# Optimization experiments

Measured on AMD Instinct MI355X. Metric: run time of the kernel, lower is better.

The kernel has to match this reference:

```python
import jax, jax.numpy as jnp
import numpy as np

B, N, D, H = 2, 2048, 1024, 16
HD = D // H  # head_dim = 64


def l2norm(x, eps=1e-12):
    n = jnp.sqrt(jnp.sum(x * x, axis=-1, keepdims=True))
    return x / jnp.maximum(n, eps)


def setup_inputs() -> dict:
    key = jax.random.key(0)
    ks = jax.random.split(key, 10)
    s = 0.02
    return {
        "x": jax.random.normal(ks[0], (B, N, D), jnp.float32),
        "Wq": jax.random.normal(ks[1], (D, D), jnp.float32) * s,
        "Wk": jax.random.normal(ks[2], (D, D), jnp.float32) * s,
        "Wv": jax.random.normal(ks[3], (D, D), jnp.float32) * s,
        "Wgamma": jax.random.normal(ks[4], (D, H), jnp.float32) * s,
        "Wf": jax.random.normal(ks[5], (D, H), jnp.float32) * s,
        "Wg1": jax.random.normal(ks[6], (D, HD), jnp.float32) * s,
        "Wg2": jax.random.normal(ks[7], (HD, D), jnp.float32) * s,
        "Wo": jax.random.normal(ks[8], (D, D), jnp.float32) * s,
        "norm_w": jnp.ones((D,), jnp.float32),
    }


def dplr_delta_rule(q, k, v, a, gk):
    # q,k,v,a,gk: (B,N,H,HD). State S: (B,H,Dk,Dv). b-vector == k here.
    # S' = S * exp(gk_t); S_t = S' + k_t (x) (a_t @ S' + v_t); o_t = q_t @ S_t
    qm, km, vm, am, gm = (jnp.moveaxis(t, 1, 0) for t in (q, k, v, a, gk))

    def step(S, inp):
        qt, kt, vt, at, gkt = inp  # (B,H,HD)
        Sp = S * jnp.exp(gkt)[..., None]
        u = jnp.einsum('bhk,bhkv->bhv', at, Sp) + vt
        S = Sp + jnp.einsum('bhk,bhv->bhkv', kt, u)
        o = jnp.einsum('bhk,bhkv->bhv', qt, S)
        return S, o

    S0 = jnp.zeros((q.shape[0], q.shape[2], q.shape[3], v.shape[3]), q.dtype)
    _, o = jax.lax.scan(step, S0, (qm, km, vm, am, gm))
    return jnp.moveaxis(o, 0, 1)  # (B,N,H,HD)


def _forward(x, Wq, Wk, Wv, Wgamma, Wf, Wg1, Wg2, Wo, norm_w):
    b, n, d = x.shape
    silu = jax.nn.silu
    q = silu(x @ Wq)
    k = silu(x @ Wk)
    v = silu(x @ Wv)
    log_f = jax.nn.log_sigmoid(x @ Wf)          # (b,n,H) scalar decay per head
    gamma = -jax.nn.sigmoid(x @ Wgamma)         # (b,n,H), 'pos' activation
    q = q.reshape(b, n, H, HD)
    k = l2norm(k.reshape(b, n, H, HD))
    v = v.reshape(b, n, H, HD)
    gk = jnp.broadcast_to(log_f[..., None], (b, n, H, HD))  # repeat over head_dim
    a = k * gamma[..., None] * jnp.exp(gk)
    out = dplr_delta_rule(q, k, v, a, gk)       # scale=1
    out = out.reshape(b, n, d)
    gate = jax.nn.sigmoid((x @ Wg1) @ Wg2)
    out = out * gate
    # LayerNorm (weight only, no bias)
    mu = jnp.mean(out, axis=-1, keepdims=True)
    var = jnp.mean(jnp.square(out - mu), axis=-1, keepdims=True)
    out = (out - mu) * jax.lax.rsqrt(var + 1e-5) * norm_w
    return out @ Wo


def reference(x, Wq, Wk, Wv, Wgamma, Wf, Wg1, Wg2, Wo, norm_w):
    return _forward(x, Wq, Wk, Wv, Wgamma, Wf, Wg1, Wg2, Wo, norm_w)
```

## Files before the change

kernel.cpp:

```cpp
#include <hip/hip_runtime.h>

#define BB 2
#define NN 2048
#define DD 1024
#define HH 16
#define HD 64
#define RR (BB * NN)
#define CT 32
#define NC (NN / CT)

typedef __bf16 bf16x8 __attribute__((ext_vector_type(8)));
typedef __bf16 bf16x4 __attribute__((ext_vector_type(4)));
typedef float f32x4 __attribute__((ext_vector_type(4)));
typedef float f32x2 __attribute__((ext_vector_type(2)));

__device__ __forceinline__ float sigmoidf_(float x) { return 1.f / (1.f + __expf(-x)); }

#define MFMA16(a, b, c) __builtin_amdgcn_mfma_f32_16x16x32_bf16((a), (b), (c), 0, 0, 0)

__device__ __forceinline__ void gl2lds16(const void* g, void* l) {
    __builtin_amdgcn_global_load_lds((const __attribute__((address_space(1))) void*)g,
                                     (__attribute__((address_space(3))) void*)l, 16, 0, 0);
}

__global__ __launch_bounds__(256) void xcvt(const float* __restrict__ x,
                                            __bf16* __restrict__ xb) {
    const size_t i = ((size_t)blockIdx.x * 256 + threadIdx.x) * 8;
    float4 a = *(const float4*)(x + i);
    float4 b = *(const float4*)(x + i + 4);
    bf16x8 o;
    o[0] = (__bf16)a.x; o[1] = (__bf16)a.y; o[2] = (__bf16)a.z; o[3] = (__bf16)a.w;
    o[4] = (__bf16)b.x; o[5] = (__bf16)b.y; o[6] = (__bf16)b.z; o[7] = (__bf16)b.w;
    *(bf16x8*)(xb + i) = o;
}

__global__ __launch_bounds__(256) void wtrans(const float* S0, const float* S1,
                                              const float* S2, const float* S3,
                                              __bf16* D0, __bf16* D1,
                                              __bf16* D2, __bf16* D3,
                                              int K, int N) {
    __shared__ float t[64][65];
    const int z = blockIdx.z;
    const float* S = (z == 0) ? S0 : ((z == 1) ? S1 : ((z == 2) ? S2 : S3));
    __bf16* D = (z == 0) ? D0 : ((z == 1) ? D1 : ((z == 2) ? D2 : D3));
    const int tid = threadIdx.x;
    const int ti = blockIdx.y * 64;
    const int tj = blockIdx.x * 64;
    const int r = tid >> 2, c0 = (tid & 3) * 16;
    const float* sp = S + (size_t)(ti + r) * N + tj + c0;
#pragma unroll
    for (int p = 0; p < 4; p++) {
        float4 v = *(const float4*)(sp + 4 * p);
        t[r][c0 + 4 * p + 0] = v.x; t[r][c0 + 4 * p + 1] = v.y;
        t[r][c0 + 4 * p + 2] = v.z; t[r][c0 + 4 * p + 3] = v.w;
    }
    __syncthreads();
    bf16x8 o0, o1;
#pragma unroll
    for (int j = 0; j < 8; j++) o0[j] = (__bf16)t[c0 + j][r];
#pragma unroll
    for (int j = 0; j < 8; j++) o1[j] = (__bf16)t[c0 + 8 + j][r];
    __bf16* dp = D + (size_t)(tj + r) * K + ti + c0;
    *(bf16x8*)dp = o0;
    *(bf16x8*)(dp + 8) = o1;
}

__global__ __launch_bounds__(256) void wtrans96(const float* __restrict__ Wgm,
                                                const float* __restrict__ Wf,
                                                const float* __restrict__ Wg1,
                                                __bf16* __restrict__ W96T) {
    const int c = blockIdx.x;
    const int k0 = threadIdx.x * 4;
    bf16x4 o;
    if (c < 96) {
        const float* src;
        int stride;
        if (c < 16)      { src = Wgm + c;        stride = 16; }
        else if (c < 32) { src = Wf + (c - 16);  stride = 16; }
        else             { src = Wg1 + (c - 32); stride = 64; }
#pragma unroll
        for (int j = 0; j < 4; j++) o[j] = (__bf16)src[(size_t)(k0 + j) * stride];
    } else {
        o[0] = o[1] = o[2] = o[3] = (__bf16)0.f;
    }
    *(bf16x4*)(W96T + (size_t)c * 1024 + k0) = o;
}

__global__ __launch_bounds__(256) void gemm_bt(const __bf16* __restrict__ A,
                                               const __bf16* B0, const __bf16* B1,
                                               const __bf16* B2, const __bf16* B3,
                                               float* C0, float* C1, float* C2, float* C3,
                                               int M, int N, int K) {
    constexpr int BK = 32;
    __shared__ __align__(16) __bf16 As[128 * BK];
    __shared__ __align__(16) __bf16 Bs[128 * BK];
    const int nwg = (int)(gridDim.x * gridDim.y);
    const int flat = (int)(blockIdx.y * gridDim.x + blockIdx.x);
    const int swz = (flat & 7) * (nwg >> 3) + (flat >> 3);
    const int bxs = swz % (int)gridDim.x, bys = swz / (int)gridDim.x;
    const int mat = bxs >> 3;
    const __bf16* B = (mat == 0) ? B0 : ((mat == 1) ? B1 : ((mat == 2) ? B2 : B3));
    float* C = (mat == 0) ? C0 : ((mat == 1) ? C1 : ((mat == 2) ? C2 : C3));
    const int Nn = (mat == 3) ? 128 : N;
    const int tid = threadIdx.x;
    const int lane = tid & 63;
    const int wave = tid >> 6;
    const int wm = (wave >> 1) * 64, wn = (wave & 1) * 64;
    const int bm = bys * 128, bn = (bxs & 7) * 128;
    const int l15 = lane & 15, quad = lane >> 4;

    const int srow = lane >> 2, scol = (lane & 3) * 8;
    const __bf16* gA = A + (size_t)(bm + wave * 16 + srow) * K + scol;
    const __bf16* gB = B + (size_t)(bn + wave * 16 + srow) * K + scol;
    const size_t rstep = (size_t)64 * K;
    __bf16* lA0 = &As[(wave * 16) * BK];
    __bf16* lA1 = &As[(wave * 16 + 64) * BK];
    __bf16* lB0 = &Bs[(wave * 16) * BK];
    __bf16* lB1 = &Bs[(wave * 16 + 64) * BK];

    f32x4 acc[4][4];
#pragma unroll
    for (int i = 0; i < 4; i++)
#pragma unroll
        for (int j = 0; j < 4; j++) acc[i][j] = (f32x4){0.f, 0.f, 0.f, 0.f};

    gl2lds16(gA, lA0);
    gl2lds16(gA + rstep, lA1);
    gl2lds16(gB, lB0);
    gl2lds16(gB + rstep, lB1);

    for (int kb = 0; kb < K; kb += BK) {
        asm volatile("s_waitcnt vmcnt(0)" ::: "memory");
        __syncthreads();

        bf16x8 af[4], bfr[4];
#pragma unroll
        for (int i = 0; i < 4; i++)
            af[i] = *(const bf16x8*)&As[(wm + i * 16 + l15) * BK + quad * 8];
#pragma unroll
        for (int j = 0; j < 4; j++)
            bfr[j] = *(const bf16x8*)&Bs[(wn + j * 16 + l15) * BK + quad * 8];
        __syncthreads();

        if (kb + BK < K) {
            gl2lds16(gA + kb + BK, lA0);
            gl2lds16(gA + kb + BK + rstep, lA1);
            gl2lds16(gB + kb + BK, lB0);
            gl2lds16(gB + kb + BK + rstep, lB1);
        }
        __builtin_amdgcn_sched_barrier(0);

#pragma unroll
        for (int i = 0; i < 4; i++)
#pragma unroll
            for (int j = 0; j < 4; j++)
                acc[i][j] = MFMA16(af[i], bfr[j], acc[i][j]);
    }

#pragma unroll
    for (int i = 0; i < 4; i++) {
#pragma unroll
        for (int r = 0; r < 4; r++) {
            const int row = bm + wm + i * 16 + quad * 4 + r;
            float* cp = C + (size_t)row * Nn + bn + wn + l15;
#pragma unroll
            for (int j = 0; j < 4; j++) cp[j * 16] = acc[i][j][r];
        }
    }
}

__global__ __launch_bounds__(256) void scal_prep(const float* __restrict__ c96,
                                                 float* __restrict__ lfb,
                                                 float* __restrict__ csb,
                                                 __bf16* __restrict__ g1b) {
    const int tid = threadIdx.x;
    const int row = blockIdx.x * 16 + (tid >> 4);
    const int h = tid & 15;
    const float* cr = c96 + (size_t)row * 128;
    const float sig = sigmoidf_(cr[16 + h]);
    const float gm = -sigmoidf_(cr[h]);
    lfb[(size_t)row * HH + h] = sig;
    csb[(size_t)row * HH + h] = gm * sig * sig;
    const int c4 = h * 4;
    bf16x4 o;
    o[0] = (__bf16)cr[32 + c4 + 0]; o[1] = (__bf16)cr[32 + c4 + 1];
    o[2] = (__bf16)cr[32 + c4 + 2]; o[3] = (__bf16)cr[32 + c4 + 3];
    *(bf16x4*)(g1b + (size_t)row * 64 + c4) = o;
}

__global__ __launch_bounds__(64) void chunk_prep(const float* __restrict__ qb,
                                                 const float* __restrict__ kb,
                                                 const float* __restrict__ lfb,
                                                 const float* __restrict__ csb,
                                                 __bf16* __restrict__ ck_hat,
                                                 __bf16* __restrict__ ck_q,
                                                 __bf16* __restrict__ ck_kbT,
                                                 __bf16* __restrict__ ck_M,
                                                 __bf16* __restrict__ ck_G,
                                                 float* __restrict__ ck_lam) {
    __shared__ __align__(16) __bf16 khL[32][72];
    __shared__ __align__(16) __bf16 kbL[32][72];
    __shared__ __align__(16) __bf16 qtL[32][72];
    __shared__ float Afp[32][33];
    __shared__ float scl[3][32];
    const int bx = blockIdx.x;
    const int bh = bx >> 6, ci = bx & 63;
    const int b = bh >> 4, h = bh & 15;
    const int l = threadIdx.x;
    const int l15 = l & 15, quad = l >> 4, t32 = l & 31;
    const size_t cid = (size_t)bh * NC + ci;

    const size_t mb = ((size_t)(b * NN + ci * CT) + t32) * HH + h;
    float c_t = csb[mb];
    float p = lfb[mb];
#pragma unroll
    for (int d = 1; d <= 16; d <<= 1) {
        float o = __shfl_up(p, d);
        p *= (t32 >= d) ? o : 1.f;
    }
    float pm1 = __shfl_up(p, 1);
    if (t32 == 0) pm1 = 1.f;
    const float lamT = __shfl(p, 31);
    if (l < 32) {
        scl[0][t32] = c_t * pm1;
        scl[1][t32] = 1.f / p;
        scl[2][t32] = p;
    }
    if (l == 0) ck_lam[cid] = lamT;
    __syncthreads();

    const size_t rb0 = ((size_t)(b * NN + ci * CT)) * DD + h * HD;
    __bf16* khG = ck_hat + cid * 2048;
    __bf16* qtG = ck_q + cid * 2048;
    __bf16* kTG = ck_kbT + cid * 2048;
#pragma unroll
    for (int rep = 0; rep < 8; rep++) {
        const int row = rep * 4 + quad;
        const int c4 = l15 * 4;
        float4 kv = *(const float4*)(kb + rb0 + (size_t)row * DD + c4);
        float4 qv = *(const float4*)(qb + rb0 + (size_t)row * DD + c4);
        kv.x *= sigmoidf_(kv.x); kv.y *= sigmoidf_(kv.y);
        kv.z *= sigmoidf_(kv.z); kv.w *= sigmoidf_(kv.w);
        qv.x *= sigmoidf_(qv.x); qv.y *= sigmoidf_(qv.y);
        qv.z *= sigmoidf_(qv.z); qv.w *= sigmoidf_(qv.w);
        float ss = kv.x * kv.x + kv.y * kv.y + kv.z * kv.z + kv.w * kv.w;
        ss += __shfl_xor(ss, 1); ss += __shfl_xor(ss, 2);
        ss += __shfl_xor(ss, 4); ss += __shfl_xor(ss, 8);
        const float inv = 1.f / fmaxf(sqrtf(ss), 1e-12f);
        const float sh = scl[0][row] * inv, sbr = scl[1][row] * inv, sq = scl[2][row];
        bf16x4 khv, kbv, qtv;
        khv[0] = (__bf16)(kv.x * sh); khv[1] = (__bf16)(kv.y * sh);
        khv[2] = (__bf16)(kv.z * sh); khv[3] = (__bf16)(kv.w * sh);
        kbv[0] = (__bf16)(kv.x * sbr); kbv[1] = (__bf16)(kv.y * sbr);
        kbv[2] = (__bf16)(kv.z * sbr); kbv[3] = (__bf16)(kv.w * sbr);
        qtv[0] = (__bf16)(qv.x * sq); qtv[1] = (__bf16)(qv.y * sq);
        qtv[2] = (__bf16)(qv.z * sq); qtv[3] = (__bf16)(qv.w * sq);
        *(bf16x4*)&khL[row][c4] = khv;
        *(bf16x4*)&kbL[row][c4] = kbv;
        *(bf16x4*)&qtL[row][c4] = qtv;
        *(bf16x4*)(khG + row * 64 + c4) = khv;
        *(bf16x4*)(qtG + row * 64 + c4) = qtv;
#pragma unroll
        for (int j = 0; j < 4; j++) kTG[(c4 + j) * 32 + row] = kbv[j];
    }
    __syncthreads();

    __bf16* GG = ck_G + cid * 1024;
#pragma unroll
    for (int mi = 0; mi < 2; mi++)
#pragma unroll
        for (int ni = 0; ni < 2; ni++) {
            f32x4 aA = (f32x4){0.f, 0.f, 0.f, 0.f};
            f32x4 aG = (f32x4){0.f, 0.f, 0.f, 0.f};
#pragma unroll
            for (int k2 = 0; k2 < 2; k2++) {
                bf16x8 bfr = *(const bf16x8*)&kbL[ni * 16 + l15][k2 * 32 + quad * 8];
                bf16x8 afr = *(const bf16x8*)&khL[mi * 16 + l15][k2 * 32 + quad * 8];
                bf16x8 qfr = *(const bf16x8*)&qtL[mi * 16 + l15][k2 * 32 + quad * 8];
                aA = MFMA16(afr, bfr, aA);
                aG = MFMA16(qfr, bfr, aG);
            }
#pragma unroll
            for (int r = 0; r < 4; r++) {
                const int row = mi * 16 + quad * 4 + r, col = ni * 16 + l15;
                Afp[row][col] = (col < row) ? aA[r] : 0.f;
                GG[row * 32 + col] = (__bf16)((col <= row) ? aG[r] : 0.f);
            }
        }
    __syncthreads();

    __bf16* MG = ck_M + cid * 1024;
    if (l < 32) {
        float m[32];
#pragma unroll
        for (int t = 0; t < 32; t++) {
            float r = (l == t) ? 1.f : 0.f;
#pragma unroll
            for (int s = 0; s < t; s++) r += Afp[t][s] * m[s];
            m[t] = r;
            MG[t * 32 + l] = (__bf16)r;
        }
    }
}

struct FragSet {
    bf16x8 ka[2][2], qa[2][2], ma[2], ga[2], kba[4];
    f32x4 vv[2];
    float lam;
};

__global__ __launch_bounds__(64, 1) void chunk_scan(const __bf16* __restrict__ ck_hat,
                                                    const __bf16* __restrict__ ck_q,
                                                    const __bf16* __restrict__ ck_kbT,
                                                    const __bf16* __restrict__ ck_M,
                                                    const __bf16* __restrict__ ck_G,
                                                    const float* __restrict__ ck_lam,
                                                    const float* __restrict__ vb,
                                                    __bf16* __restrict__ obh) {
    __shared__ __align__(16) __bf16 Sbt[16][72];
    __shared__ __align__(16) __bf16 Vbt[16][40];
    __shared__ __align__(16) __bf16 Ubt[16][40];
    const int bx = blockIdx.x;
    const int bh = bx >> 2, vs = bx & 3;
    const int b = bh >> 4, h = bh & 15;
    const int l = threadIdx.x, l15 = l & 15, quad = l >> 4;
    const size_t cid0 = (size_t)bh * NC;
    const size_t vcol = (size_t)h * HD + vs * 16 + l15;
    const size_t rowb = (size_t)b * NN;

    f32x4 S[4];
#pragma unroll
    for (int dt = 0; dt < 4; dt++) S[dt] = (f32x4){0.f, 0.f, 0.f, 0.f};

    auto load = [&](FragSet& f, int ci) {
        const __bf16* khp = ck_hat + (cid0 + ci) * 2048;
        const __bf16* qp = ck_q + (cid0 + ci) * 2048;
        const __bf16* kTp = ck_kbT + (cid0 + ci) * 2048;
        const __bf16* Mp = ck_M + (cid0 + ci) * 1024;
        const __bf16* Gp = ck_G + (cid0 + ci) * 1024;
#pragma unroll
        for (int mi = 0; mi < 2; mi++) {
#pragma unroll
            for (int k2 = 0; k2 < 2; k2++) {
                f.ka[mi][k2] = *(const bf16x8*)(khp + (mi * 16 + l15) * 64 + k2 * 32 + quad * 8);
                f.qa[mi][k2] = *(const bf16x8*)(qp + (mi * 16 + l15) * 64 + k2 * 32 + quad * 8);
            }
            f.ma[mi] = *(const bf16x8*)(Mp + (mi * 16 + l15) * 32 + quad * 8);
            f.ga[mi] = *(const bf16x8*)(Gp + (mi * 16 + l15) * 32 + quad * 8);
        }
#pragma unroll
        for (int dt = 0; dt < 4; dt++)
            f.kba[dt] = *(const bf16x8*)(kTp + (dt * 16 + l15) * 32 + quad * 8);
#pragma unroll
        for (int mi = 0; mi < 2; mi++)
#pragma unroll
            for (int r = 0; r < 4; r++)
                f.vv[mi][r] = vb[(rowb + ci * CT + mi * 16 + quad * 4 + r) * DD + vcol];
        f.lam = ck_lam[cid0 + ci];
    };

    auto compute = [&](const FragSet& f, int ci) {
        const f32x4 z = (f32x4){0.f, 0.f, 0.f, 0.f};
#pragma unroll
        for (int dt = 0; dt < 4; dt++) {
            bf16x4 t;
#pragma unroll
            for (int r = 0; r < 4; r++) t[r] = (__bf16)S[dt][r];
            *(bf16x4*)&Sbt[l15][dt * 16 + quad * 4] = t;
        }
        bf16x8 sb0 = *(const bf16x8*)&Sbt[l15][quad * 8];
        bf16x8 sb1 = *(const bf16x8*)&Sbt[l15][32 + quad * 8];
        f32x4 p0 = MFMA16(f.ka[0][0], sb0, z); p0 = MFMA16(f.ka[0][1], sb1, p0);
        f32x4 p1 = MFMA16(f.ka[1][0], sb0, z); p1 = MFMA16(f.ka[1][1], sb1, p1);
#pragma unroll
        for (int r = 0; r < 4; r++) {
            const float v0 = f.vv[0][r], v1 = f.vv[1][r];
            p0[r] += v0 * sigmoidf_(v0);
            p1[r] += v1 * sigmoidf_(v1);
        }
        bf16x4 t0, t1;
#pragma unroll
        for (int r = 0; r < 4; r++) { t0[r] = (__bf16)p0[r]; t1[r] = (__bf16)p1[r]; }
        *(bf16x4*)&Vbt[l15][quad * 4] = t0;
        *(bf16x4*)&Vbt[l15][16 + quad * 4] = t1;
        bf16x8 vfr = *(const bf16x8*)&Vbt[l15][quad * 8];
        f32x4 u0 = MFMA16(f.ma[0], vfr, z);
        f32x4 u1 = MFMA16(f.ma[1], vfr, z);
#pragma unroll
        for (int r = 0; r < 4; r++) { t0[r] = (__bf16)u0[r]; t1[r] = (__bf16)u1[r]; }
        *(bf16x4*)&Ubt[l15][quad * 4] = t0;
        *(bf16x4*)&Ubt[l15][16 + quad * 4] = t1;
        bf16x8 ufr = *(const bf16x8*)&Ubt[l15][quad * 8];
        f32x4 o0 = MFMA16(f.qa[0][0], sb0, z); o0 = MFMA16(f.qa[0][1], sb1, o0);
        o0 = MFMA16(f.ga[0], ufr, o0);
        f32x4 o1 = MFMA16(f.qa[1][0], sb0, z); o1 = MFMA16(f.qa[1][1], sb1, o1);
        o1 = MFMA16(f.ga[1], ufr, o1);
#pragma unroll
        for (int r = 0; r < 4; r++) {
            obh[(rowb + ci * CT + quad * 4 + r) * DD + vcol] = (__bf16)o0[r];
            obh[(rowb + ci * CT + 16 + quad * 4 + r) * DD + vcol] = (__bf16)o1[r];
        }
#pragma unroll
        for (int dt = 0; dt < 4; dt++) {
            S[dt] = MFMA16(f.kba[dt], ufr, S[dt]);
#pragma unroll
            for (int r = 0; r < 4; r++) S[dt][r] *= f.lam;
        }
    };

    FragSet fA, fB;
    load(fA, 0);
    for (int ci = 0; ci < NC; ci += 2) {
        load(fB, ci + 1);
        __builtin_amdgcn_sched_barrier(0);
        compute(fA, ci);
        load(fA, (ci + 2 < NC) ? ci + 2 : NC - 1);
        __builtin_amdgcn_sched_barrier(0);
        compute(fB, ci + 1);
    }
}

__global__ __launch_bounds__(256) void gate_ln_kernel(const __bf16* __restrict__ obh,
                                                      const float* __restrict__ gatep,
                                                      const float* __restrict__ nw,
                                                      __bf16* __restrict__ lnob) {
    const int r = blockIdx.x, tid = threadIdx.x;
    const int wav = tid >> 6, lane = tid & 63;
    __shared__ float red[8];
    const size_t rb = (size_t)r * DD;

    float vals[4];
    float s = 0.f;
#pragma unroll
    for (int p = 0; p < 4; p++) {
        const int j = tid + 256 * p;
        float xg = (float)obh[rb + j] * sigmoidf_(gatep[rb + j]);
        vals[p] = xg;
        s += xg;
    }
#pragma unroll
    for (int m = 1; m <= 32; m <<= 1) s += __shfl_xor(s, m);
    if (lane == 0) red[wav] = s;
    __syncthreads();
    const float mu = (red[0] + red[1] + red[2] + red[3]) * (1.f / 1024.f);

    float s2 = 0.f;
#pragma unroll
    for (int p = 0; p < 4; p++) { float d = vals[p] - mu; s2 += d * d; }
#pragma unroll
    for (int m = 1; m <= 32; m <<= 1) s2 += __shfl_xor(s2, m);
    if (lane == 0) red[4 + wav] = s2;
    __syncthreads();
    const float var = (red[4] + red[5] + red[6] + red[7]) * (1.f / 1024.f);
    const float rs = rsqrtf(var + 1e-5f);

#pragma unroll
    for (int p = 0; p < 4; p++) {
        const int j = tid + 256 * p;
        lnob[rb + j] = (__bf16)((vals[p] - mu) * rs * nw[j]);
    }
}

extern "C" void kernel_launch(void* const* d_in, const int* in_sizes, int n_in,
                              void* d_out, int out_size, void* d_ws, size_t ws_size,
                              hipStream_t stream) {
    const float* x   = (const float*)d_in[0];
    const float* Wq  = (const float*)d_in[1];
    const float* Wk  = (const float*)d_in[2];
    const float* Wv  = (const float*)d_in[3];
    const float* Wgm = (const float*)d_in[4];
    const float* Wf  = (const float*)d_in[5];
    const float* Wg1 = (const float*)d_in[6];
    const float* Wg2 = (const float*)d_in[7];
    const float* Wo  = (const float*)d_in[8];
    const float* nw  = (const float*)d_in[9];
    float* out = (float*)d_out;

    float* w = (float*)d_ws;
    float* qb    = w;
    float* kb    = qb + 4194304;
    float* vb    = kb + 4194304;
    float* gatep = vb + 4194304;
    __bf16* g1b  = (__bf16*)(gatep + 4194304);
    float* lfb   = gatep + 4194304 + 131072;
    float* csb   = lfb + 65536;
    __bf16* obh  = (__bf16*)(csb + 65536);
    float* cw    = csb + 65536 + 2097152;
    __bf16* ck_hat = (__bf16*)cw;
    __bf16* ck_q   = (__bf16*)(cw + 2097152);
    __bf16* ck_kbT = (__bf16*)(cw + 4194304);
    __bf16* ck_M   = (__bf16*)(cw + 6291456);
    __bf16* ck_G   = (__bf16*)(cw + 7340032);
    float*  ck_lam = cw + 8388608;
    float* nw2   = cw + 8390656;
    __bf16* xb   = (__bf16*)nw2;
    __bf16* WqT  = (__bf16*)(nw2 + 2097152);
    __bf16* WkT  = (__bf16*)(nw2 + 2621440);
    __bf16* WvT  = (__bf16*)(nw2 + 3145728);
    __bf16* WoT  = (__bf16*)(nw2 + 3670016);
    __bf16* Wg2T = (__bf16*)(nw2 + 4194304);
    __bf16* W96T = (__bf16*)(nw2 + 4227072);
    float* c96   = nw2 + 4292608;
    __bf16* lnob = (__bf16*)qb;

    dim3 blk(256);
    xcvt<<<2048, blk, 0, stream>>>(x, xb);
    wtrans<<<dim3(16, 16, 4), blk, 0, stream>>>(Wq, Wk, Wv, Wo, WqT, WkT, WvT, WoT,
                                                DD, DD);
    wtrans<<<dim3(16, 1, 1), blk, 0, stream>>>(Wg2, Wg2, Wg2, Wg2, Wg2T, Wg2T, Wg2T,
                                               Wg2T, HD, DD);
    wtrans96<<<128, blk, 0, stream>>>(Wgm, Wf, Wg1, W96T);
    gemm_bt<<<dim3(25, 32), blk, 0, stream>>>(xb, WqT, WkT, WvT, W96T,
                                              qb, kb, vb, c96, RR, DD, DD);
    scal_prep<<<RR / 16, blk, 0, stream>>>(c96, lfb, csb, g1b);
    gemm_bt<<<dim3(8, 32), blk, 0, stream>>>(g1b, Wg2T, Wg2T, Wg2T, Wg2T,
                                             gatep, gatep, gatep, gatep, RR, DD, HD);
    chunk_prep<<<32 * NC, 64, 0, stream>>>(qb, kb, lfb, csb,
                                           ck_hat, ck_q, ck_kbT, ck_M, ck_G, ck_lam);
    chunk_scan<<<128, 64, 0, stream>>>(ck_hat, ck_q, ck_kbT, ck_M, ck_G, ck_lam, vb, obh);
    gate_ln_kernel<<<RR, blk, 0, stream>>>(obh, gatep, nw, lnob);
    gemm_bt<<<dim3(8, 32), blk, 0, stream>>>(lnob, WoT, WoT, WoT, WoT,
                                             out, out, out, out, RR, DD, DD);
}
```

Baseline: 257.7 us.

## Precompute M·K̂ and M·V per chunk in prep to shorten the sequential scan

After: 241.8 us. 6.2% less time.

```diff
diff --git a/kernel.cpp b/kernel.cpp
--- a/kernel.cpp
+++ b/kernel.cpp
@@ -190,17 +190,21 @@
 
 __global__ __launch_bounds__(64) void chunk_prep(const float* __restrict__ qb,
                                                  const float* __restrict__ kb,
+                                                 const float* __restrict__ vb,
                                                  const float* __restrict__ lfb,
                                                  const float* __restrict__ csb,
-                                                 __bf16* __restrict__ ck_hat,
+                                                 __bf16* __restrict__ ck_mkh,
                                                  __bf16* __restrict__ ck_q,
                                                  __bf16* __restrict__ ck_kbT,
-                                                 __bf16* __restrict__ ck_M,
                                                  __bf16* __restrict__ ck_G,
+                                                 __bf16* __restrict__ ck_uvT,
                                                  float* __restrict__ ck_lam) {
     __shared__ __align__(16) __bf16 khL[32][72];
     __shared__ __align__(16) __bf16 kbL[32][72];
     __shared__ __align__(16) __bf16 qtL[32][72];
+    __shared__ __align__(16) __bf16 khT[64][40];
+    __shared__ __align__(16) __bf16 vsT[64][40];
+    __shared__ __align__(16) __bf16 Ms[32][40];
     __shared__ float Afp[32][33];
     __shared__ float scl[3][32];
     const int bx = blockIdx.x;
@@ -230,7 +234,6 @@
     __syncthreads();
 
     const size_t rb0 = ((size_t)(b * NN + ci * CT)) * DD + h * HD;
-    __bf16* khG = ck_hat + cid * 2048;
     __bf16* qtG = ck_q + cid * 2048;
     __bf16* kTG = ck_kbT + cid * 2048;
 #pragma unroll
@@ -239,10 +242,13 @@
         const int c4 = l15 * 4;
         float4 kv = *(const float4*)(kb + rb0 + (size_t)row * DD + c4);
         float4 qv = *(const float4*)(qb + rb0 + (size_t)row * DD + c4);
+        float4 vv = *(const float4*)(vb + rb0 + (size_t)row * DD + c4);
         kv.x *= sigmoidf_(kv.x); kv.y *= sigmoidf_(kv.y);
         kv.z *= sigmoidf_(kv.z); kv.w *= sigmoidf_(kv.w);
         qv.x *= sigmoidf_(qv.x); qv.y *= sigmoidf_(qv.y);
         qv.z *= sigmoidf_(qv.z); qv.w *= sigmoidf_(qv.w);
+        vv.x *= sigmoidf_(vv.x); vv.y *= sigmoidf_(vv.y);
+        vv.z *= sigmoidf_(vv.z); vv.w *= sigmoidf_(vv.w);
         float ss = kv.x * kv.x + kv.y * kv.y + kv.z * kv.z + kv.w * kv.w;
         ss += __shfl_xor(ss, 1); ss += __shfl_xor(ss, 2);
         ss += __shfl_xor(ss, 4); ss += __shfl_xor(ss, 8);
@@ -258,10 +264,14 @@
         *(bf16x4*)&khL[row][c4] = khv;
         *(bf16x4*)&kbL[row][c4] = kbv;
         *(bf16x4*)&qtL[row][c4] = qtv;
-        *(bf16x4*)(khG + row * 64 + c4) = khv;
         *(bf16x4*)(qtG + row * 64 + c4) = qtv;
 #pragma unroll
-        for (int j = 0; j < 4; j++) kTG[(c4 + j) * 32 + row] = kbv[j];
+        for (int j = 0; j < 4; j++) {
+            kTG[(c4 + j) * 32 + row] = kbv[j];
+            khT[c4 + j][row] = khv[j];
+        }
+        vsT[c4 + 0][row] = (__bf16)vv.x; vsT[c4 + 1][row] = (__bf16)vv.y;
+        vsT[c4 + 2][row] = (__bf16)vv.z; vsT[c4 + 3][row] = (__bf16)vv.w;
     }
     __syncthreads();
 
@@ -289,7 +299,6 @@
         }
     __syncthreads();
 
-    __bf16* MG = ck_M + cid * 1024;
     if (l < 32) {
         float m[32];
 #pragma unroll
@@ -298,27 +307,47 @@
 #pragma unroll
             for (int s = 0; s < t; s++) r += Afp[t][s] * m[s];
             m[t] = r;
-            MG[t * 32 + l] = (__bf16)r;
+            Ms[t][l] = (__bf16)r;
+        }
+    }
+    __syncthreads();
+
+    const f32x4 z = (f32x4){0.f, 0.f, 0.f, 0.f};
+    __bf16* mkhG = ck_mkh + cid * 2048;
+    __bf16* uvTG = ck_uvT + cid * 2048;
+#pragma unroll
+    for (int mi = 0; mi < 2; mi++) {
+        bf16x8 am = *(const bf16x8*)&Ms[mi * 16 + l15][quad * 8];
+#pragma unroll
+        for (int ni = 0; ni < 4; ni++) {
+            bf16x8 bk = *(const bf16x8*)&khT[ni * 16 + l15][quad * 8];
+            bf16x8 bv = *(const bf16x8*)&vsT[ni * 16 + l15][quad * 8];
+            f32x4 aM = MFMA16(am, bk, z);
+            f32x4 aV = MFMA16(am, bv, z);
+#pragma unroll
+            for (int r = 0; r < 4; r++) {
+                const int trow = mi * 16 + quad * 4 + r, col = ni * 16 + l15;
+                mkhG[trow * 64 + col] = (__bf16)aM[r];
+                uvTG[col * 32 + trow] = (__bf16)aV[r];
+            }
         }
     }
 }
 
 struct FragSet {
-    bf16x8 ka[2][2], qa[2][2], ma[2], ga[2], kba[4];
-    f32x4 vv[2];
+    bf16x8 mkha[2][2], qa[2][2], ga[2], kba[4];
+    bf16x4 uvb[2];
     float lam;
 };
 
-__global__ __launch_bounds__(64, 1) void chunk_scan(const __bf16* __restrict__ ck_hat,
-                                                    const __bf16* __restrict__ ck_q,
-                                                    const __bf16* __restrict__ ck_kbT,
-                                                    const __bf16* __restrict__ ck_M,
-                                                    const __bf16* __restrict__ ck_G,
-                                                    const float* __restrict__ ck_lam,
-                                                    const float* __restrict__ vb,
-                                                    __bf16* __restrict__ obh) {
+__global__ __launch_bounds__(64) void chunk_scan(const __bf16* __restrict__ ck_mkh,
+                                                 const __bf16* __restrict__ ck_q,
+                                                 const __bf16* __restrict__ ck_kbT,
+                                                 const __bf16* __restrict__ ck_G,
+                                                 const __bf16* __restrict__ ck_uvT,
+                                                 const float* __restrict__ ck_lam,
+                                                 __bf16* __restrict__ obh) {
     __shared__ __align__(16) __bf16 Sbt[16][72];
-    __shared__ __align__(16) __bf16 Vbt[16][40];
     __shared__ __align__(16) __bf16 Ubt[16][40];
     const int bx = blockIdx.x;
     const int bh = bx >> 2, vs = bx & 3;
@@ -333,29 +362,24 @@
     for (int dt = 0; dt < 4; dt++) S[dt] = (f32x4){0.f, 0.f, 0.f, 0.f};
 
     auto load = [&](FragSet& f, int ci) {
-        const __bf16* khp = ck_hat + (cid0 + ci) * 2048;
+        const __bf16* mkp = ck_mkh + (cid0 + ci) * 2048;
         const __bf16* qp = ck_q + (cid0 + ci) * 2048;
         const __bf16* kTp = ck_kbT + (cid0 + ci) * 2048;
-        const __bf16* Mp = ck_M + (cid0 + ci) * 1024;
         const __bf16* Gp = ck_G + (cid0 + ci) * 1024;
+        const __bf16* uvp = ck_uvT + (cid0 + ci) * 2048;
 #pragma unroll
         for (int mi = 0; mi < 2; mi++) {
 #pragma unroll
             for (int k2 = 0; k2 < 2; k2++) {
-                f.ka[mi][k2] = *(const bf16x8*)(khp + (mi * 16 + l15) * 64 + k2 * 32 + quad * 8);
+                f.mkha[mi][k2] = *(const bf16x8*)(mkp + (mi * 16 + l15) * 64 + k2 * 32 + quad * 8);
                 f.qa[mi][k2] = *(const bf16x8*)(qp + (mi * 16 + l15) * 64 + k2 * 32 + quad * 8);
             }
-            f.ma[mi] = *(const bf16x8*)(Mp + (mi * 16 + l15) * 32 + quad * 8);
             f.ga[mi] = *(const bf16x8*)(Gp + (mi * 16 + l15) * 32 + quad * 8);
+            f.uvb[mi] = *(const bf16x4*)(uvp + (vs * 16 + l15) * 32 + mi * 16 + quad * 4);
         }
 #pragma unroll
         for (int dt = 0; dt < 4; dt++)
             f.kba[dt] = *(const bf16x8*)(kTp + (dt * 16 + l15) * 32 + quad * 8);
-#pragma unroll
-        for (int mi = 0; mi < 2; mi++)
-#pragma unroll
-            for (int r = 0; r < 4; r++)
-                f.vv[mi][r] = vb[(rowb + ci * CT + mi * 16 + quad * 4 + r) * DD + vcol];
         f.lam = ck_lam[cid0 + ci];
     };
 
@@ -370,22 +394,14 @@
         }
         bf16x8 sb0 = *(const bf16x8*)&Sbt[l15][quad * 8];
         bf16x8 sb1 = *(const bf16x8*)&Sbt[l15][32 + quad * 8];
-        f32x4 p0 = MFMA16(f.ka[0][0], sb0, z); p0 = MFMA16(f.ka[0][1], sb1, p0);
-        f32x4 p1 = MFMA16(f.ka[1][0], sb0, z); p1 = MFMA16(f.ka[1][1], sb1, p1);
+        f32x4 u0 = MFMA16(f.mkha[0][0], sb0, z); u0 = MFMA16(f.mkha[0][1], sb1, u0);
+        f32x4 u1 = MFMA16(f.mkha[1][0], sb0, z); u1 = MFMA16(f.mkha[1][1], sb1, u1);
 #pragma unroll
         for (int r = 0; r < 4; r++) {
-            const float v0 = f.vv[0][r], v1 = f.vv[1][r];
-            p0[r] += v0 * sigmoidf_(v0);
-            p1[r] += v1 * sigmoidf_(v1);
+            u0[r] += (float)f.uvb[0][r];
+            u1[r] += (float)f.uvb[1][r];
         }
         bf16x4 t0, t1;
-#pragma unroll
-        for (int r = 0; r < 4; r++) { t0[r] = (__bf16)p0[r]; t1[r] = (__bf16)p1[r]; }
-        *(bf16x4*)&Vbt[l15][quad * 4] = t0;
-        *(bf16x4*)&Vbt[l15][16 + quad * 4] = t1;
-        bf16x8 vfr = *(const bf16x8*)&Vbt[l15][quad * 8];
-        f32x4 u0 = MFMA16(f.ma[0], vfr, z);
-        f32x4 u1 = MFMA16(f.ma[1], vfr, z);
 #pragma unroll
         for (int r = 0; r < 4; r++) { t0[r] = (__bf16)u0[r]; t1[r] = (__bf16)u1[r]; }
         *(bf16x4*)&Ubt[l15][quad * 4] = t0;
@@ -486,13 +502,13 @@
     float* csb   = lfb + 65536;
     __bf16* obh  = (__bf16*)(csb + 65536);
     float* cw    = csb + 65536 + 2097152;
-    __bf16* ck_hat = (__bf16*)cw;
+    __bf16* ck_mkh = (__bf16*)cw;
     __bf16* ck_q   = (__bf16*)(cw + 2097152);
     __bf16* ck_kbT = (__bf16*)(cw + 4194304);
-    __bf16* ck_M   = (__bf16*)(cw + 6291456);
-    __bf16* ck_G   = (__bf16*)(cw + 7340032);
-    float*  ck_lam = cw + 8388608;
-    float* nw2   = cw + 8390656;
+    __bf16* ck_G   = (__bf16*)(cw + 6291456);
+    __bf16* ck_uvT = (__bf16*)(cw + 7340032);
+    float*  ck_lam = cw + 9437184;
+    float* nw2   = cw + 9439232;
     __bf16* xb   = (__bf16*)nw2;
     __bf16* WqT  = (__bf16*)(nw2 + 2097152);
     __bf16* WkT  = (__bf16*)(nw2 + 2621440);
@@ -515,9 +531,9 @@
     scal_prep<<<RR / 16, blk, 0, stream>>>(c96, lfb, csb, g1b);
     gemm_bt<<<dim3(8, 32), blk, 0, stream>>>(g1b, Wg2T, Wg2T, Wg2T, Wg2T,
                                              gatep, gatep, gatep, gatep, RR, DD, HD);
-    chunk_prep<<<32 * NC, 64, 0, stream>>>(qb, kb, lfb, csb,
-                                           ck_hat, ck_q, ck_kbT, ck_M, ck_G, ck_lam);
-    chunk_scan<<<128, 64, 0, stream>>>(ck_hat, ck_q, ck_kbT, ck_M, ck_G, ck_lam, vb, obh);
+    chunk_prep<<<32 * NC, 64, 0, stream>>>(qb, kb, vb, lfb, csb,
+                                           ck_mkh, ck_q, ck_kbT, ck_G, ck_uvT, ck_lam);
+    chunk_scan<<<128, 64, 0, stream>>>(ck_mkh, ck_q, ck_kbT, ck_G, ck_uvT, ck_lam, obh);
     gate_ln_kernel<<<RR, blk, 0, stream>>>(obh, gatep, nw, lnob);
     gemm_bt<<<dim3(8, 32), blk, 0, stream>>>(lnob, WoT, WoT, WoT, WoT,
                                              out, out, out, out, RR, DD, DD);
```
